# Performance work log

Hardware: AMD Instinct MI355X
Metric: run time of the kernel (lower is better)

The kernel has to match this reference:

```python
import jax, jax.numpy as jnp
import numpy as np
from jax import lax

D_MODEL = 1024
D_STATE = 16
D_CONV = 4
EXPAND = 2
D_INNER = EXPAND * D_MODEL          # 2048
DT_RANK = (D_MODEL + 15) // 16      # 64


def setup_inputs() -> dict:
    key = jax.random.key(0)
    ks = jax.random.split(key, 12)
    B, L = 2, 2048
    s = lambda *sh: 1.0 / np.sqrt(sh[-1])
    inp = {
        "x": jax.random.normal(ks[0], (B, L, D_MODEL), jnp.float32),
        "in_proj_w": jax.random.normal(ks[1], (2 * D_INNER, D_MODEL), jnp.float32) * s(0, D_MODEL),
        "conv_w": jax.random.normal(ks[2], (D_INNER, 1, D_CONV), jnp.float32) * s(0, D_CONV),
        "conv_b": jax.random.normal(ks[3], (D_INNER,), jnp.float32) * 0.01,
        "x_proj_w": jax.random.normal(ks[4], (DT_RANK + 2 * D_STATE, D_INNER), jnp.float32) * s(0, D_INNER),
        "dt_proj_w": jax.random.normal(ks[5], (D_INNER, DT_RANK), jnp.float32) * s(0, DT_RANK),
        "dt_proj_b": jax.random.normal(ks[6], (D_INNER,), jnp.float32) * 0.1 - 4.0,  # softplus(dt) small
        "A_log": jnp.log(jnp.broadcast_to(jnp.arange(1, D_STATE + 1, dtype=jnp.float32), (D_INNER, D_STATE))),
        "D": jnp.ones((D_INNER,), jnp.float32),
        "out_proj_w": jax.random.normal(ks[7], (D_MODEL, D_INNER), jnp.float32) * s(0, D_INNER),
        "ln_w": jnp.ones((D_MODEL,), jnp.float32),
        "ln_b": jnp.zeros((D_MODEL,), jnp.float32),
    }
    return inp


def _mamba(x, in_proj_w, conv_w, conv_b, x_proj_w, dt_proj_w, dt_proj_b, A_log, D, out_proj_w):
    B, L, _ = x.shape
    xz = jnp.einsum("bld,ed->ble", x, in_proj_w)          # [B,L,2*d_inner]
    xi, z = jnp.split(xz, 2, axis=-1)                       # each [B,L,d_inner]

    # causal depthwise conv1d over time
    xt = jnp.transpose(xi, (0, 2, 1))                       # [B,d_inner,L]
    xc = lax.conv_general_dilated(
        xt, conv_w, window_strides=(1,), padding=[(D_CONV - 1, 0)],
        dimension_numbers=("NCH", "OIH", "NCH"), feature_group_count=D_INNER)
    xc = jax.nn.silu(xc + conv_b[None, :, None])            # [B,d_inner,L]
    u = jnp.transpose(xc, (0, 2, 1))                        # [B,L,d_inner]

    x_dbl = jnp.einsum("bld,ed->ble", u, x_proj_w)          # [B,L,dt_rank+2N]
    dt, Bm, Cm = jnp.split(x_dbl, [DT_RANK, DT_RANK + D_STATE], axis=-1)
    delta = jax.nn.softplus(jnp.einsum("blr,dr->bld", dt, dt_proj_w) + dt_proj_b)  # [B,L,d_inner]

    A = -jnp.exp(A_log)                                     # [d_inner,N]

    def step(h, inputs):
        d_t, B_t, C_t, u_t = inputs                         # [B,d], [B,N], [B,N], [B,d]
        dA = jnp.exp(d_t[..., None] * A)                    # [B,d_inner,N]
        h = dA * h + (d_t * u_t)[..., None] * B_t[:, None, :]
        y_t = jnp.einsum("bdn,bn->bd", h, C_t)
        return h, y_t

    xs = (jnp.transpose(delta, (1, 0, 2)), jnp.transpose(Bm, (1, 0, 2)),
          jnp.transpose(Cm, (1, 0, 2)), jnp.transpose(u, (1, 0, 2)))
    h0 = jnp.zeros((B, D_INNER, D_STATE), x.dtype)
    _, ys = lax.scan(step, h0, xs)                          # ys [L,B,d_inner]
    y = jnp.transpose(ys, (1, 0, 2)) + u * D                # skip connection
    y = y * jax.nn.silu(z)                                  # gate
    return jnp.einsum("bld,ed->ble", y, out_proj_w)         # [B,L,d_model]


def reference(x, in_proj_w, conv_w, conv_b, x_proj_w, dt_proj_w, dt_proj_b,
              A_log, D, out_proj_w, ln_w, ln_b):
    residual = x
    y = _mamba(x, in_proj_w, conv_w, conv_b, x_proj_w, dt_proj_w, dt_proj_b,
               A_log, D, out_proj_w)
    # dropout is identity in eval; residual + LayerNorm
    h = y + residual
    mu = jnp.mean(h, axis=-1, keepdims=True)
    var = jnp.var(h, axis=-1, keepdims=True)
    return (h - mu) * lax.rsqrt(var + 1e-5) * ln_w + ln_b
```

## Files before the change

kernel.cpp:

```cpp
#include <hip/hip_runtime.h>

typedef unsigned short u16;
typedef __attribute__((ext_vector_type(8))) short bf8_t;
typedef __attribute__((ext_vector_type(4))) float f4_t;
typedef __attribute__((ext_vector_type(4))) unsigned short u16x4;
typedef __attribute__((ext_vector_type(8))) unsigned short u16x8;

__device__ __forceinline__ float b2f(u16 h) {
  union { unsigned u; float f; } v; v.u = ((unsigned)h) << 16; return v.f;
}
__device__ __forceinline__ u16 f2b(float f) {
  union { float f; unsigned u; } v; v.f = f;
  unsigned u = v.u;
  u += 0x7fffu + ((u >> 16) & 1u);
  return (u16)(u >> 16);
}

#define AS1C(p) ((const __attribute__((address_space(1))) void*)(p))
#define AS3(p)  ((__attribute__((address_space(3))) void*)(p))

__global__ __launch_bounds__(256)
void cvt_all(const float* __restrict__ x, const float* __restrict__ inW,
             const float* __restrict__ xprojW, const float* __restrict__ dtW,
             const float* __restrict__ outW,
             u16* __restrict__ xb, u16* __restrict__ inWb, u16* __restrict__ xpb,
             u16* __restrict__ dtWb, u16* __restrict__ outWb)
{
  int i = blockIdx.x * 256 + threadIdx.x;
  if (i >= 2703360) return;
  const float* s; u16* d; int off;
  if (i < 1048576)      { s = x;      d = xb;    off = i; }
  else if (i < 2097152) { s = inW;    d = inWb;  off = i - 1048576; }
  else if (i < 2146304) { s = xprojW; d = xpb;   off = i - 2097152; }
  else if (i < 2179072) { s = dtW;    d = dtWb;  off = i - 2146304; }
  else                  { s = outW;   d = outWb; off = i - 2179072; }
  f4_t v = *(const f4_t*)(s + (size_t)off * 4);
  u16x4 o;
#pragma unroll
  for (int j = 0; j < 4; ++j) o[j] = f2b(v[j]);
  *(u16x4*)(d + (size_t)off * 4) = o;
}

__device__ __forceinline__ void stage64(const u16* g, int ld, int row0, int rowmax,
                                        int k0, u16* lds, int wid, int lane) {
  int qg = (lane & 7) ^ ((lane >> 3) & 7);
#pragma unroll
  for (int c = 0; c < 4; ++c) {
    int chunk = wid * 4 + c;
    int r = row0 + chunk * 8 + (lane >> 3);
    if (r > rowmax) r = rowmax;
    const u16* gp = g + (size_t)r * ld + k0 + qg * 8;
    __builtin_amdgcn_global_load_lds(AS1C(gp), AS3(lds + chunk * 512), 16, 0, 0);
  }
}

template<int EPI>
__device__ __forceinline__ void gemm_body(const u16* __restrict__ A, int lda,
             const u16* __restrict__ Bt, int ldb,
             int Kblk, int Nact,
             u16* __restrict__ o16, float* __restrict__ of32,
             float* __restrict__ of32b, const float* __restrict__ biasf)
{
  __shared__ u16 lsA[128 * 64];
  __shared__ u16 lsB[128 * 64];
  const int tid = threadIdx.x;
  const int wid = tid >> 6, lane = tid & 63;
  const int wm = wid >> 1, wn = wid & 1;
  const int lrow = lane & 15;
  const int kq = lane >> 4;
  const int sw = lrow & 7;
  const int m0 = blockIdx.y * 128;
  const int n0 = (EPI == 1) ? 0 : blockIdx.x * 128;
  int kbase = 0;
  if (EPI == 1) kbase = blockIdx.x * Kblk;
  if (EPI == 3) kbase = blockIdx.z * Kblk;

  f4_t acc[4][4];
#pragma unroll
  for (int i = 0; i < 4; ++i)
#pragma unroll
    for (int j = 0; j < 4; ++j) acc[i][j] = {0.f, 0.f, 0.f, 0.f};

  for (int kt = kbase; kt < kbase + Kblk; kt += 64) {
    stage64(A,  lda, m0, 0x3fffffff, kt, lsA, wid, lane);
    stage64(Bt, ldb, n0, Nact - 1,   kt, lsB, wid, lane);
    __syncthreads();
#pragma unroll
    for (int h = 0; h < 2; ++h) {
      const int lk = ((h * 4 + kq) ^ sw) * 8;
      bf8_t af[4], bfr[4];
#pragma unroll
      for (int mi = 0; mi < 4; ++mi)
        af[mi] = *(const bf8_t*)&lsA[(wm * 64 + mi * 16 + lrow) * 64 + lk];
#pragma unroll
      for (int ni = 0; ni < 4; ++ni)
        bfr[ni] = *(const bf8_t*)&lsB[(wn * 64 + ni * 16 + lrow) * 64 + lk];
#pragma unroll
      for (int mi = 0; mi < 4; ++mi)
#pragma unroll
        for (int ni = 0; ni < 4; ++ni)
          acc[mi][ni] = __builtin_amdgcn_mfma_f32_16x16x32_bf16(af[mi], bfr[ni], acc[mi][ni], 0, 0, 0);
    }
    __syncthreads();
  }

  const int rq = (lane >> 4) * 4;
#pragma unroll
  for (int mi = 0; mi < 4; ++mi) {
#pragma unroll
    for (int ni = 0; ni < 4; ++ni) {
#pragma unroll
      for (int r = 0; r < 4; ++r) {
        int m = m0 + wm * 64 + mi * 16 + rq + r;
        int n = n0 + wn * 64 + ni * 16 + lrow;
        float v = acc[mi][ni][r];
        if (EPI == 1) {
          if (n < 96) of32[((size_t)blockIdx.x * 4096 + m) * 96 + n] = v;
        } else if (EPI == 2) {
          float t = v + biasf[n];
          float sp = (t > 20.f) ? t : log1pf(__expf(t));
          o16[(size_t)m * 2048 + n] = f2b(sp);
        } else {
          float* dst = blockIdx.z ? of32b : of32;
          dst[(size_t)m * 1024 + n] = v;
        }
      }
    }
  }
}

__global__ __launch_bounds__(256)
void gemm_xp(const u16* A, int lda, const u16* Bt, int ldb, int Kblk, int Nact,
             u16* o16, float* of32, float* of32b, const float* biasf)
{ gemm_body<1>(A, lda, Bt, ldb, Kblk, Nact, o16, of32, of32b, biasf); }

__global__ __launch_bounds__(256)
void gemm_dt(const u16* A, int lda, const u16* Bt, int ldb, int Kblk, int Nact,
             u16* o16, float* of32, float* of32b, const float* biasf)
{ gemm_body<2>(A, lda, Bt, ldb, Kblk, Nact, o16, of32, of32b, biasf); }

__global__ __launch_bounds__(256)
void gemm_out(const u16* A, int lda, const u16* Bt, int ldb, int Kblk, int Nact,
              u16* o16, float* of32, float* of32b, const float* biasf)
{ gemm_body<3>(A, lda, Bt, ldb, Kblk, Nact, o16, of32, of32b, biasf); }


__device__ __forceinline__ void stageu(const u16* __restrict__ g, int ld,
                                       int row0, int k0, u16* ldsu,
                                       int wid, int lane) {
  int qg = (lane & 7) ^ ((lane >> 3) & 7);
#pragma unroll
  for (int j = 0; j < 2; ++j) {
    int rr = j * 64 + wid * 8 + (lane >> 3);
    const u16* gp = g + (size_t)(row0 + rr) * ld + k0 + qg * 8;
    __builtin_amdgcn_global_load_lds(AS1C(gp), AS3(ldsu + (j * 512 + wid * 64) * 8), 16, 0, 0);
  }
}

#define G8_BAR()   __builtin_amdgcn_s_barrier()
#define G8_LGKM0() do { asm volatile("s_waitcnt lgkmcnt(0)" ::: "memory"); \
                        __builtin_amdgcn_sched_barrier(0); } while (0)
#define G8_LGKM8() asm volatile("s_waitcnt lgkmcnt(8)" ::: "memory")
#define G8_VM(N)   do { asm volatile("s_waitcnt vmcnt(" #N ")" ::: "memory"); \
                        __builtin_amdgcn_sched_barrier(0); } while (0)

#define RD_A(base, MH) do { \
  _Pragma("unroll") \
  for (int mi_ = 0; mi_ < 4; ++mi_) { \
    af[mi_][0] = *(const bf8_t*)((base) + arow + ((MH) * 64 + mi_ * 16) * 64 + aq0); \
    af[mi_][1] = *(const bf8_t*)((base) + arow + ((MH) * 64 + mi_ * 16) * 64 + aq1); \
  } } while (0)

#define RD_B(base, NH) do { \
  _Pragma("unroll") \
  for (int ni_ = 0; ni_ < 2; ++ni_) { \
    bfr[NH][ni_][0] = *(const bf8_t*)((base) + brow + ((NH) * 32 + ni_ * 16) * 64 + aq0); \
    bfr[NH][ni_][1] = *(const bf8_t*)((base) + brow + ((NH) * 32 + ni_ * 16) * 64 + aq1); \
  } } while (0)

#define MMA(MH, NH) do { \
  __builtin_amdgcn_s_setprio(1); \
  _Pragma("unroll") \
  for (int mi_ = 0; mi_ < 4; ++mi_) \
    _Pragma("unroll") \
    for (int ni_ = 0; ni_ < 2; ++ni_) { \
      acc[(MH) * 4 + mi_][(NH) * 2 + ni_] = __builtin_amdgcn_mfma_f32_16x16x32_bf16( \
          af[mi_][0], bfr[NH][ni_][0], acc[(MH) * 4 + mi_][(NH) * 2 + ni_], 0, 0, 0); \
      acc[(MH) * 4 + mi_][(NH) * 2 + ni_] = __builtin_amdgcn_mfma_f32_16x16x32_bf16( \
          af[mi_][1], bfr[NH][ni_][1], acc[(MH) * 4 + mi_][(NH) * 2 + ni_], 0, 0, 0); \
    } \
  __builtin_amdgcn_s_setprio(0); \
} while (0)

__global__ __launch_bounds__(512, 2)
void gemm8_in(const u16* __restrict__ A, const u16* __restrict__ Bt,
              u16* __restrict__ o16)
{
  __shared__ u16 ls[65536];
  const int tid = threadIdx.x;
  const int wid = tid >> 6, lane = tid & 63;
  const int wm = wid >> 2, wn = wid & 3;
  const int lrow = lane & 15;
  const int kq = lane >> 4;
  const int sw = lrow & 7;
  const int m0 = blockIdx.y * 256;
  const int n0 = blockIdx.x * 256;
  u16* lsA0 = ls;
  u16* lsB0 = ls + 16384;
  u16* lsA1 = ls + 32768;
  u16* lsB1 = ls + 49152;
  const int arow = (wm * 128 + lrow) * 64;
  const int brow = (wn * 64 + lrow) * 64;
  const int aq0 = (kq ^ sw) * 8;
  const int aq1 = ((4 + kq) ^ sw) * 8;

  f4_t acc[8][4];
#pragma unroll
  for (int i = 0; i < 8; ++i)
#pragma unroll
    for (int j = 0; j < 4; ++j) acc[i][j] = {0.f, 0.f, 0.f, 0.f};
  bf8_t af[4][2];
  bf8_t bfr[2][2][2];

  stageu(A,  1024, m0,        0, lsA0,        wid, lane);
  stageu(A,  1024, m0 + 128,  0, lsA0 + 8192, wid, lane);
  stageu(Bt, 1024, n0,        0, lsB0,        wid, lane);
  stageu(Bt, 1024, n0 + 128,  0, lsB0 + 8192, wid, lane);
  stageu(Bt, 1024, n0,       64, lsB1,        wid, lane);
  stageu(Bt, 1024, n0 + 128, 64, lsB1 + 8192, wid, lane);
  G8_VM(4); G8_BAR();

#pragma unroll 1
  for (int i = 0; i < 7; ++i) {
    const int k1 = (2 * i + 1) * 64, k2 = k1 + 64, k3 = k1 + 128;
    RD_A(lsA0, 0); RD_B(lsB0, 0);
    stageu(A, 1024, m0, k1, lsA1, wid, lane);
    G8_LGKM8(); G8_BAR(); G8_LGKM0(); MMA(0, 0); G8_BAR();
    RD_B(lsB0, 1);
    stageu(A, 1024, m0 + 128, k1, lsA1 + 8192, wid, lane);
    G8_BAR(); G8_LGKM0(); MMA(0, 1); G8_BAR();
    RD_A(lsA0, 1);
    stageu(Bt, 1024, n0, k2, lsB0, wid, lane);
    G8_BAR(); G8_LGKM0(); MMA(1, 0); G8_BAR();
    stageu(Bt, 1024, n0 + 128, k2, lsB0 + 8192, wid, lane);
    G8_BAR(); G8_LGKM0(); MMA(1, 1); G8_VM(4); G8_BAR();
    RD_A(lsA1, 0); RD_B(lsB1, 0);
    stageu(A, 1024, m0, k2, lsA0, wid, lane);
    G8_LGKM8(); G8_BAR(); G8_LGKM0(); MMA(0, 0); G8_BAR();
    RD_B(lsB1, 1);
    stageu(A, 1024, m0 + 128, k2, lsA0 + 8192, wid, lane);
    G8_BAR(); G8_LGKM0(); MMA(0, 1); G8_BAR();
    RD_A(lsA1, 1);
    stageu(Bt, 1024, n0, k3, lsB1, wid, lane);
    G8_BAR(); G8_LGKM0(); MMA(1, 0); G8_BAR();
    stageu(Bt, 1024, n0 + 128, k3, lsB1 + 8192, wid, lane);
    G8_BAR(); G8_LGKM0(); MMA(1, 1); G8_VM(4); G8_BAR();
  }

  {
    const int k1 = 960;
    RD_A(lsA0, 0); RD_B(lsB0, 0);
    stageu(A, 1024, m0, k1, lsA1, wid, lane);
    G8_LGKM8(); G8_BAR(); G8_LGKM0(); MMA(0, 0); G8_BAR();
    RD_B(lsB0, 1);
    stageu(A, 1024, m0 + 128, k1, lsA1 + 8192, wid, lane);
    G8_BAR(); G8_LGKM0(); MMA(0, 1); G8_BAR();
    RD_A(lsA0, 1);
    G8_BAR(); G8_LGKM0(); MMA(1, 0); G8_BAR();
    G8_BAR(); G8_LGKM0(); MMA(1, 1); G8_VM(0); G8_BAR();
    RD_A(lsA1, 0); RD_B(lsB1, 0);
    G8_BAR(); G8_LGKM0(); MMA(0, 0); G8_BAR();
    RD_B(lsB1, 1);
    G8_BAR(); G8_LGKM0(); MMA(0, 1); G8_BAR();
    RD_A(lsA1, 1);
    G8_BAR(); G8_LGKM0(); MMA(1, 0); G8_BAR();
    G8_LGKM0(); MMA(1, 1);
  }

  const int rq = (lane >> 4) * 4;
#pragma unroll
  for (int mi = 0; mi < 8; ++mi) {
#pragma unroll
    for (int ni = 0; ni < 4; ++ni) {
#pragma unroll
      for (int r = 0; r < 4; ++r) {
        int m = m0 + wm * 128 + mi * 16 + rq + r;
        int n = n0 + wn * 64 + ni * 16 + lrow;
        float v = acc[mi][ni][r];
        if (n < 2048) o16[(size_t)m * 2048 + n] = f2b(v);
        else          o16[(size_t)8388608 + (size_t)m * 2048 + (n - 2048)] = f2b(v);
      }
    }
  }
}

__global__ __launch_bounds__(256)
void xproj_reduce(const float* __restrict__ part, u16* __restrict__ dtA,
                  float* __restrict__ bc)
{
  int idx = blockIdx.x * 256 + threadIdx.x;
  int m = idx / 96, n = idx - m * 96;
  float s = 0.f;
#pragma unroll
  for (int p = 0; p < 8; ++p) s += part[(size_t)p * 393216 + idx];
  if (n < 64) dtA[(size_t)m * 64 + n] = f2b(s);
  else        bc[(size_t)m * 32 + (n - 64)] = s;
}

__global__ __launch_bounds__(256)
void conv_silu(const u16* __restrict__ xib, const float* __restrict__ cw,
               const float* __restrict__ cb, u16* __restrict__ ub)
{
  int i = blockIdx.x * 256 + threadIdx.x;
  int c8 = (i & 255) * 8;
  int row = i >> 8;
  int l = row & 2047;
  const u16* base = xib + (size_t)row * 2048 + c8;
  u16x8 x0 = {0,0,0,0,0,0,0,0}, x1 = x0, x2 = x0, x3;
  x3 = *(const u16x8*)(base);
  if (l >= 1) x2 = *(const u16x8*)(base - 2048);
  if (l >= 2) x1 = *(const u16x8*)(base - 2 * 2048);
  if (l >= 3) x0 = *(const u16x8*)(base - 3 * 2048);
  f4_t cb0 = *(const f4_t*)(cb + c8);
  f4_t cb1 = *(const f4_t*)(cb + c8 + 4);
  u16x8 o;
#pragma unroll
  for (int j = 0; j < 8; ++j) {
    f4_t w = *(const f4_t*)(cw + (size_t)(c8 + j) * 4);
    float a = (j < 4 ? cb0[j] : cb1[j - 4])
            + w[0] * b2f(x0[j]) + w[1] * b2f(x1[j])
            + w[2] * b2f(x2[j]) + w[3] * b2f(x3[j]);
    float s = a / (1.f + __expf(-a));
    o[j] = f2b(s);
  }
  *(u16x8*)(ub + (size_t)row * 2048 + c8) = o;
}

__global__ __launch_bounds__(256)
void scan_s1(const u16* __restrict__ delta_bf, const u16* __restrict__ ub,
             const float* __restrict__ bc, const float* __restrict__ alog,
             u16* __restrict__ S, float* __restrict__ Q)
{
  int blk = blockIdx.x;
  int g = blk & 7, c = (blk >> 3) & 63, b = blk >> 9;
  int d = g * 256 + threadIdx.x;
  float Av[16];
#pragma unroll
  for (int nq = 0; nq < 4; ++nq) {
    f4_t al = *(const f4_t*)(alog + (size_t)d * 16 + nq * 4);
#pragma unroll
    for (int j = 0; j < 4; ++j) Av[nq * 4 + j] = -__expf(al[j]);
  }
  float Av0 = Av[0];
  bool st = true;
#pragma unroll
  for (int n = 1; n < 16; ++n)
    st = st && (fabsf(Av[n] - (float)(n + 1) * Av0) <= 1e-3f * (float)(n + 1));
  f4_t Qr[4];
#pragma unroll
  for (int nq = 0; nq < 4; ++nq) Qr[nq] = {0.f,0.f,0.f,0.f};
  float Sd = 0.f;
  int row0 = b * 2048 + c * 32;
  if (st) {
#pragma unroll 2
    for (int i = 0; i < 32; ++i) {
      size_t row = (size_t)(row0 + i);
      float dlt = b2f(delta_bf[row * 2048 + d]);
      float uv  = b2f(ub[row * 2048 + d]);
      const float* bp = bc + row * 32;
      f4_t Bv[4];
#pragma unroll
      for (int nq = 0; nq < 4; ++nq) Bv[nq] = *(const f4_t*)(bp + nq * 4);
      float du = dlt * uv;
      float e1 = __expf(dlt * Av0);
      float a = e1;
      Sd += dlt;
#pragma unroll
      for (int n = 0; n < 16; ++n) {
        Qr[n >> 2][n & 3] = a * Qr[n >> 2][n & 3] + du * Bv[n >> 2][n & 3];
        a *= e1;
      }
    }
  } else {
#pragma unroll 2
    for (int i = 0; i < 32; ++i) {
      size_t row = (size_t)(row0 + i);
      float dlt = b2f(delta_bf[row * 2048 + d]);
      float uv  = b2f(ub[row * 2048 + d]);
      const float* bp = bc + row * 32;
      f4_t Bv[4];
#pragma unroll
      for (int nq = 0; nq < 4; ++nq) Bv[nq] = *(const f4_t*)(bp + nq * 4);
      float du = dlt * uv;
      Sd += dlt;
#pragma unroll
      for (int n = 0; n < 16; ++n) {
        float a = __expf(dlt * Av[n]);
        Qr[n >> 2][n & 3] = a * Qr[n >> 2][n & 3] + du * Bv[n >> 2][n & 3];
      }
    }
  }
  S[(size_t)(b * 64 + c) * 2048 + d] = f2b(Sd);
  size_t o = ((size_t)((b * 64 + c) * 2048 + d)) * 16;
#pragma unroll
  for (int nq = 0; nq < 4; ++nq)
    *(f4_t*)(Q + o + nq * 4) = Qr[nq];
}

__global__ __launch_bounds__(256)
void scan_comb(const u16* __restrict__ S16, float* __restrict__ Q,
               const float* __restrict__ alog)
{
  int idx = blockIdx.x * 256 + threadIdx.x;
  int b = idx >> 15, dn = idx & 32767;
  int d = dn >> 4;
  float Av = -__expf(alog[dn]);
  size_t qbase = (size_t)b * 2097152 + dn;
  size_t sbase = (size_t)b * 131072 + d;
  float H = 0.f;
#pragma unroll
  for (int cg = 0; cg < 4; ++cg) {
    float sv[16], qv[16];
#pragma unroll
    for (int j = 0; j < 16; ++j) {
      int c = cg * 16 + j;
      qv[j] = Q[qbase + (size_t)c * 32768];
      sv[j] = b2f(S16[sbase + (size_t)c * 2048]);
    }
#pragma unroll
    for (int j = 0; j < 16; ++j) {
      int c = cg * 16 + j;
      Q[qbase + (size_t)c * 32768] = H;
      H = __expf(Av * sv[j]) * H + qv[j];
    }
  }
}

__global__ __launch_bounds__(256)
void scan_s3(const u16* __restrict__ delta_bf, const u16* __restrict__ ub,
             const float* __restrict__ bc, const float* __restrict__ alog,
             const float* __restrict__ Q, const float* __restrict__ Dw,
             u16* __restrict__ zy)
{
  int blk = blockIdx.x;
  int g = blk & 7, c = (blk >> 3) & 63, b = blk >> 9;
  int d = g * 256 + threadIdx.x;
  float Av[16];
#pragma unroll
  for (int nq = 0; nq < 4; ++nq) {
    f4_t al = *(const f4_t*)(alog + (size_t)d * 16 + nq * 4);
#pragma unroll
    for (int j = 0; j < 4; ++j) Av[nq * 4 + j] = -__expf(al[j]);
  }
  float Av0 = Av[0];
  bool st = true;
#pragma unroll
  for (int n = 1; n < 16; ++n)
    st = st && (fabsf(Av[n] - (float)(n + 1) * Av0) <= 1e-3f * (float)(n + 1));
  f4_t h4[4];
  size_t o = ((size_t)((b * 64 + c) * 2048 + d)) * 16;
#pragma unroll
  for (int nq = 0; nq < 4; ++nq) h4[nq] = *(const f4_t*)(Q + o + nq * 4);
  float Dv = Dw[d];
  int row0 = b * 2048 + c * 32;
  if (st) {
#pragma unroll 2
    for (int i = 0; i < 32; ++i) {
      size_t row = (size_t)(row0 + i);
      float dlt = b2f(delta_bf[row * 2048 + d]);
      float uv  = b2f(ub[row * 2048 + d]);
      const float* bp = bc + row * 32;
      f4_t Bv[4], Cv[4];
#pragma unroll
      for (int nq = 0; nq < 4; ++nq) { Bv[nq] = *(const f4_t*)(bp + nq * 4); Cv[nq] = *(const f4_t*)(bp + 16 + nq * 4); }
      float du = dlt * uv;
      float e1 = __expf(dlt * Av0);
      float a = e1;
      float y = 0.f;
#pragma unroll
      for (int n = 0; n < 16; ++n) {
        float hn = a * h4[n >> 2][n & 3] + du * Bv[n >> 2][n & 3];
        h4[n >> 2][n & 3] = hn;
        y += hn * Cv[n >> 2][n & 3];
        a *= e1;
      }
      float zv = b2f(zy[row * 2048 + d]);
      float ov = (y + Dv * uv) * (zv / (1.f + __expf(-zv)));
      zy[row * 2048 + d] = f2b(ov);
    }
  } else {
#pragma unroll 2
    for (int i = 0; i < 32; ++i) {
      size_t row = (size_t)(row0 + i);
      float dlt = b2f(delta_bf[row * 2048 + d]);
      float uv  = b2f(ub[row * 2048 + d]);
      const float* bp = bc + row * 32;
      f4_t Bv[4], Cv[4];
#pragma unroll
      for (int nq = 0; nq < 4; ++nq) { Bv[nq] = *(const f4_t*)(bp + nq * 4); Cv[nq] = *(const f4_t*)(bp + 16 + nq * 4); }
      float du = dlt * uv;
      float y = 0.f;
#pragma unroll
      for (int n = 0; n < 16; ++n) {
        float a = __expf(dlt * Av[n]);
        float hn = a * h4[n >> 2][n & 3] + du * Bv[n >> 2][n & 3];
        h4[n >> 2][n & 3] = hn;
        y += hn * Cv[n >> 2][n & 3];
      }
      float zv = b2f(zy[row * 2048 + d]);
      float ov = (y + Dv * uv) * (zv / (1.f + __expf(-zv)));
      zy[row * 2048 + d] = f2b(ov);
    }
  }
}

__global__ __launch_bounds__(256)
void ln_kernel(const float* __restrict__ hp0, const float* __restrict__ hp1,
               const float* __restrict__ xin,
               const float* __restrict__ lnw, const float* __restrict__ lnb,
               float* __restrict__ outp)
{
  __shared__ float ssum[4], ssq[4];
  int row = blockIdx.x, t = threadIdx.x;
  f4_t h0 = *(const f4_t*)(hp0 + (size_t)row * 1024 + t * 4);
  f4_t h1 = *(const f4_t*)(hp1 + (size_t)row * 1024 + t * 4);
  f4_t xv = *(const f4_t*)(xin + (size_t)row * 1024 + t * 4);
  float v[4], s = 0.f, q = 0.f;
#pragma unroll
  for (int j = 0; j < 4; ++j) { v[j] = h0[j] + h1[j] + xv[j]; s += v[j]; q += v[j] * v[j]; }
#pragma unroll
  for (int m = 32; m; m >>= 1) { s += __shfl_xor(s, m, 64); q += __shfl_xor(q, m, 64); }
  int wv = t >> 6;
  if ((t & 63) == 0) { ssum[wv] = s; ssq[wv] = q; }
  __syncthreads();
  s = ssum[0] + ssum[1] + ssum[2] + ssum[3];
  q = ssq[0] + ssq[1] + ssq[2] + ssq[3];
  float mu = s * (1.f / 1024.f);
  float var = q * (1.f / 1024.f) - mu * mu;
  float rs = rsqrtf(var + 1e-5f);
  f4_t o;
#pragma unroll
  for (int j = 0; j < 4; ++j)
    o[j] = (v[j] - mu) * rs * lnw[t * 4 + j] + lnb[t * 4 + j];
  *(f4_t*)(outp + (size_t)row * 1024 + t * 4) = o;
}

extern "C" void kernel_launch(void* const* d_in, const int* in_sizes, int n_in,
                              void* d_out, int out_size, void* d_ws, size_t ws_size,
                              hipStream_t stream)
{
  const float* x      = (const float*)d_in[0];
  const float* inW    = (const float*)d_in[1];
  const float* convW  = (const float*)d_in[2];
  const float* convB  = (const float*)d_in[3];
  const float* xprojW = (const float*)d_in[4];
  const float* dtW    = (const float*)d_in[5];
  const float* dtB    = (const float*)d_in[6];
  const float* alog   = (const float*)d_in[7];
  const float* Dw     = (const float*)d_in[8];
  const float* outW   = (const float*)d_in[9];
  const float* lnw    = (const float*)d_in[10];
  const float* lnb    = (const float*)d_in[11];
  float* out = (float*)d_out;

  char* ws = (char*)d_ws;
  u16*   xiz    = (u16*)(ws);
  u16*   zy     = xiz + 8388608;
  u16*   xb     = (u16*)(ws + 33554432);
  u16*   inWb   = xb + 4194304;
  u16*   u_bf   = (u16*)(ws + 33554432);
  u16*   dtA    = (u16*)(ws + 50331648);
  float* bc     = (float*)(ws + 50855936);
  u16*   xprojWb= (u16*)(ws + 51380224);
  u16*   dtWb   = (u16*)(ws + 51773440);
  u16*   outWb  = (u16*)(ws + 52035584);
  u16*   delta  = xiz;
  float* hpart1 = (float*)(ws);
  float* hpart0 = (float*)d_out;
  float* xpart  = (float*)d_out;
  u16*   Sbuf   = dtA;
  float* Qbuf   = (float*)d_out;

  dim3 blk(256);
  cvt_all<<<10560, blk, 0, stream>>>(x, inW, xprojW, dtW, outW,
                                     xb, inWb, xprojWb, dtWb, outWb);
  gemm8_in<<<dim3(16, 16), dim3(512), 0, stream>>>(xb, inWb, xiz);
  conv_silu<<<4096, blk, 0, stream>>>(xiz, convW, convB, u_bf);
  gemm_xp<<<dim3(8, 32), blk, 0, stream>>>(u_bf, 2048, xprojWb, 2048, 256, 96, nullptr, xpart, nullptr, nullptr);
  xproj_reduce<<<1536, blk, 0, stream>>>(xpart, dtA, bc);
  gemm_dt<<<dim3(16, 32), blk, 0, stream>>>(dtA, 64, dtWb, 64, 64, 2048, delta, nullptr, nullptr, dtB);
  scan_s1<<<1024, blk, 0, stream>>>(delta, u_bf, bc, alog, Sbuf, Qbuf);
  scan_comb<<<256, blk, 0, stream>>>(Sbuf, Qbuf, alog);
  scan_s3<<<1024, blk, 0, stream>>>(delta, u_bf, bc, alog, Qbuf, Dw, zy);
  gemm_out<<<dim3(8, 32, 2), blk, 0, stream>>>(zy, 2048, outWb, 2048, 1024, 1024, nullptr, hpart0, hpart1, nullptr);
  ln_kernel<<<4096, blk, 0, stream>>>(hpart0, hpart1, x, lnw, lnb, out);
}
```

Before: 311.9 us.

## Replace out-projection GEMM with double-buffered 512-thread pipelined kernel

Swaps the generic 256-thread 128x128 out-projection GEMM for a dedicated 512-thread kernel that computes a 128x256 tile. It double-buffers A and B tiles in LDS via global_load_lds and interleaves the staging of the next k-slice with the MFMA phases, raising MFMA priority with setprio. The split-K into two partial outputs is kept. This is meant to hide global-load latency and raise MFMA utilisation, at the cost of heavy LDS use (96 KB) and many barriers per iteration.

Result: no change. 310.4 us (-0.5%).

```diff
diff --git a/kernel.cpp b/kernel.cpp
--- a/kernel.cpp
+++ b/kernel.cpp
@@ -73,7 +73,6 @@
   const int n0 = (EPI == 1) ? 0 : blockIdx.x * 128;
   int kbase = 0;
   if (EPI == 1) kbase = blockIdx.x * Kblk;
-  if (EPI == 3) kbase = blockIdx.z * Kblk;
 
   f4_t acc[4][4];
 #pragma unroll
@@ -120,9 +119,6 @@
           float t = v + biasf[n];
           float sp = (t > 20.f) ? t : log1pf(__expf(t));
           o16[(size_t)m * 2048 + n] = f2b(sp);
-        } else {
-          float* dst = blockIdx.z ? of32b : of32;
-          dst[(size_t)m * 1024 + n] = v;
         }
       }
     }
@@ -138,11 +134,6 @@
 void gemm_dt(const u16* A, int lda, const u16* Bt, int ldb, int Kblk, int Nact,
              u16* o16, float* of32, float* of32b, const float* biasf)
 { gemm_body<2>(A, lda, Bt, ldb, Kblk, Nact, o16, of32, of32b, biasf); }
-
-__global__ __launch_bounds__(256)
-void gemm_out(const u16* A, int lda, const u16* Bt, int ldb, int Kblk, int Nact,
-              u16* o16, float* of32, float* of32b, const float* biasf)
-{ gemm_body<3>(A, lda, Bt, ldb, Kblk, Nact, o16, of32, of32b, biasf); }
 
 
 __device__ __forceinline__ void stageu(const u16* __restrict__ g, int ld,
@@ -294,6 +285,126 @@
   }
 }
 
+
+#define ORD_A(base, MH) do { \
+  _Pragma("unroll") \
+  for (int mi_ = 0; mi_ < 2; ++mi_) { \
+    af[mi_][0] = *(const bf8_t*)((base) + arow + ((MH) * 32 + mi_ * 16) * 64 + aq0); \
+    af[mi_][1] = *(const bf8_t*)((base) + arow + ((MH) * 32 + mi_ * 16) * 64 + aq1); \
+  } } while (0)
+
+#define OMMA(MH, NH) do { \
+  __builtin_amdgcn_s_setprio(1); \
+  _Pragma("unroll") \
+  for (int mi_ = 0; mi_ < 2; ++mi_) \
+    _Pragma("unroll") \
+    for (int ni_ = 0; ni_ < 2; ++ni_) { \
+      acc[(MH) * 2 + mi_][(NH) * 2 + ni_] = __builtin_amdgcn_mfma_f32_16x16x32_bf16( \
+          af[mi_][0], bfr[NH][ni_][0], acc[(MH) * 2 + mi_][(NH) * 2 + ni_], 0, 0, 0); \
+      acc[(MH) * 2 + mi_][(NH) * 2 + ni_] = __builtin_amdgcn_mfma_f32_16x16x32_bf16( \
+          af[mi_][1], bfr[NH][ni_][1], acc[(MH) * 2 + mi_][(NH) * 2 + ni_], 0, 0, 0); \
+    } \
+  __builtin_amdgcn_s_setprio(0); \
+} while (0)
+
+__global__ __launch_bounds__(512, 2)
+void gemm8_out(const u16* __restrict__ A, const u16* __restrict__ Bt,
+               float* __restrict__ of32, float* __restrict__ of32b)
+{
+  __shared__ u16 ls[49152];
+  const int tid = threadIdx.x;
+  const int wid = tid >> 6, lane = tid & 63;
+  const int wm = wid >> 2, wn = wid & 3;
+  const int lrow = lane & 15;
+  const int kq = lane >> 4;
+  const int sw = lrow & 7;
+  const int m0 = blockIdx.y * 128;
+  const int n0 = blockIdx.x * 256;
+  const int kbase = blockIdx.z * 1024;
+  u16* lsA0 = ls;
+  u16* lsB0 = ls + 8192;
+  u16* lsA1 = ls + 24576;
+  u16* lsB1 = ls + 32768;
+  const int arow = (wm * 64 + lrow) * 64;
+  const int brow = (wn >> 1) * 8192 + ((wn & 1) * 64 + lrow) * 64;
+  const int aq0 = (kq ^ sw) * 8;
+  const int aq1 = ((4 + kq) ^ sw) * 8;
+
+  f4_t acc[4][4];
+#pragma unroll
+  for (int i = 0; i < 4; ++i)
+#pragma unroll
+    for (int j = 0; j < 4; ++j) acc[i][j] = {0.f, 0.f, 0.f, 0.f};
+  bf8_t af[2][2];
+  bf8_t bfr[2][2][2];
+
+  stageu(A,  2048, m0,        kbase,      lsA0,        wid, lane);
+  stageu(Bt, 2048, n0,        kbase,      lsB0,        wid, lane);
+  stageu(Bt, 2048, n0 + 128,  kbase,      lsB0 + 8192, wid, lane);
+  stageu(Bt, 2048, n0,        kbase + 64, lsB1,        wid, lane);
+  stageu(Bt, 2048, n0 + 128,  kbase + 64, lsB1 + 8192, wid, lane);
+  G8_VM(4); G8_BAR();
+
+#pragma unroll 1
+  for (int i = 0; i < 7; ++i) {
+    const int k1 = kbase + (2 * i + 1) * 64, k2 = k1 + 64, k3 = k1 + 128;
+    ORD_A(lsA0, 0); RD_B(lsB0, 0);
+    stageu(A, 2048, m0, k1, lsA1, wid, lane);
+    G8_BAR(); G8_LGKM0(); OMMA(0, 0); G8_BAR();
+    RD_B(lsB0, 1);
+    G8_BAR(); G8_LGKM0(); OMMA(0, 1); G8_BAR();
+    ORD_A(lsA0, 1);
+    stageu(Bt, 2048, n0, k2, lsB0, wid, lane);
+    G8_BAR(); G8_LGKM0(); OMMA(1, 0); G8_BAR();
+    stageu(Bt, 2048, n0 + 128, k2, lsB0 + 8192, wid, lane);
+    G8_BAR(); G8_LGKM0(); OMMA(1, 1); G8_VM(4); G8_BAR();
+    ORD_A(lsA1, 0); RD_B(lsB1, 0);
+    stageu(A, 2048, m0, k2, lsA0, wid, lane);
+    G8_BAR(); G8_LGKM0(); OMMA(0, 0); G8_BAR();
+    RD_B(lsB1, 1);
+    G8_BAR(); G8_LGKM0(); OMMA(0, 1); G8_BAR();
+    ORD_A(lsA1, 1);
+    stageu(Bt, 2048, n0, k3, lsB1, wid, lane);
+    G8_BAR(); G8_LGKM0(); OMMA(1, 0); G8_BAR();
+    stageu(Bt, 2048, n0 + 128, k3, lsB1 + 8192, wid, lane);
+    G8_BAR(); G8_LGKM0(); OMMA(1, 1); G8_VM(4); G8_BAR();
+  }
+
+  {
+    const int k1 = kbase + 960;
+    ORD_A(lsA0, 0); RD_B(lsB0, 0);
+    stageu(A, 2048, m0, k1, lsA1, wid, lane);
+    G8_BAR(); G8_LGKM0(); OMMA(0, 0); G8_BAR();
+    RD_B(lsB0, 1);
+    G8_BAR(); G8_LGKM0(); OMMA(0, 1); G8_BAR();
+    ORD_A(lsA0, 1);
+    G8_BAR(); G8_LGKM0(); OMMA(1, 0); G8_BAR();
+    G8_BAR(); G8_LGKM0(); OMMA(1, 1); G8_VM(0); G8_BAR();
+    ORD_A(lsA1, 0); RD_B(lsB1, 0);
+    G8_BAR(); G8_LGKM0(); OMMA(0, 0); G8_BAR();
+    RD_B(lsB1, 1);
+    G8_BAR(); G8_LGKM0(); OMMA(0, 1); G8_BAR();
+    ORD_A(lsA1, 1);
+    G8_BAR(); G8_LGKM0(); OMMA(1, 0); G8_BAR();
+    G8_LGKM0(); OMMA(1, 1);
+  }
+
+  float* dst = blockIdx.z ? of32b : of32;
+  const int rq = (lane >> 4) * 4;
+#pragma unroll
+  for (int mi = 0; mi < 4; ++mi) {
+#pragma unroll
+    for (int ni = 0; ni < 4; ++ni) {
+#pragma unroll
+      for (int r = 0; r < 4; ++r) {
+        int m = m0 + wm * 64 + mi * 16 + rq + r;
+        int n = n0 + wn * 64 + ni * 16 + lrow;
+        dst[(size_t)m * 1024 + n] = acc[mi][ni][r];
+      }
+    }
+  }
+}
+
 __global__ __launch_bounds__(256)
 void xproj_reduce(const float* __restrict__ part, u16* __restrict__ dtA,
                   float* __restrict__ bc)
@@ -592,6 +703,6 @@
   scan_s1<<<1024, blk, 0, stream>>>(delta, u_bf, bc, alog, Sbuf, Qbuf);
   scan_comb<<<256, blk, 0, stream>>>(Sbuf, Qbuf, alog);
   scan_s3<<<1024, blk, 0, stream>>>(delta, u_bf, bc, alog, Qbuf, Dw, zy);
-  gemm_out<<<dim3(8, 32, 2), blk, 0, stream>>>(zy, 2048, outWb, 2048, 1024, 1024, nullptr, hpart0, hpart1, nullptr);
+  gemm8_out<<<dim3(4, 32, 2), dim3(512), 0, stream>>>(zy, outWb, hpart0, hpart1);
   ln_kernel<<<4096, blk, 0, stream>>>(hpart0, hpart1, x, lnw, lnb, out);
 }
```

## Replace split-K out-projection GEMM with double-buffered 512-thread pipelined GEMM

Applied to the files above, without the earlier changes.

The out-projection GEMM used a split-K of 2 with 256-thread blocks, writing two fp32 partials that the layernorm kernel then summed. It is replaced by a 512-thread, 8-wave kernel that runs the full K=2048 loop over double-buffered LDS with async global-to-LDS loads interleaved with MFMA phases and raised wave priority. This drops one fp32 partial write and read and the partial sum in layernorm. The cost is that the grid halves to 256 blocks, lowering parallelism, and correctness now depends on hand-placed waitcnt and barrier ordering.

Result: faster. 305.1 us (-2.2%).

```diff
diff --git a/kernel.cpp b/kernel.cpp
--- a/kernel.cpp
+++ b/kernel.cpp
@@ -59,7 +59,7 @@
              const u16* __restrict__ Bt, int ldb,
              int Kblk, int Nact,
              u16* __restrict__ o16, float* __restrict__ of32,
-             float* __restrict__ of32b, const float* __restrict__ biasf)
+             const float* __restrict__ biasf)
 {
   __shared__ u16 lsA[128 * 64];
   __shared__ u16 lsB[128 * 64];
@@ -73,7 +73,6 @@
   const int n0 = (EPI == 1) ? 0 : blockIdx.x * 128;
   int kbase = 0;
   if (EPI == 1) kbase = blockIdx.x * Kblk;
-  if (EPI == 3) kbase = blockIdx.z * Kblk;
 
   f4_t acc[4][4];
 #pragma unroll
@@ -120,9 +119,6 @@
           float t = v + biasf[n];
           float sp = (t > 20.f) ? t : log1pf(__expf(t));
           o16[(size_t)m * 2048 + n] = f2b(sp);
-        } else {
-          float* dst = blockIdx.z ? of32b : of32;
-          dst[(size_t)m * 1024 + n] = v;
         }
       }
     }
@@ -131,18 +127,13 @@
 
 __global__ __launch_bounds__(256)
 void gemm_xp(const u16* A, int lda, const u16* Bt, int ldb, int Kblk, int Nact,
-             u16* o16, float* of32, float* of32b, const float* biasf)
-{ gemm_body<1>(A, lda, Bt, ldb, Kblk, Nact, o16, of32, of32b, biasf); }
+             u16* o16, float* of32, const float* biasf)
+{ gemm_body<1>(A, lda, Bt, ldb, Kblk, Nact, o16, of32, biasf); }
 
 __global__ __launch_bounds__(256)
 void gemm_dt(const u16* A, int lda, const u16* Bt, int ldb, int Kblk, int Nact,
-             u16* o16, float* of32, float* of32b, const float* biasf)
-{ gemm_body<2>(A, lda, Bt, ldb, Kblk, Nact, o16, of32, of32b, biasf); }
-
-__global__ __launch_bounds__(256)
-void gemm_out(const u16* A, int lda, const u16* Bt, int ldb, int Kblk, int Nact,
-              u16* o16, float* of32, float* of32b, const float* biasf)
-{ gemm_body<3>(A, lda, Bt, ldb, Kblk, Nact, o16, of32, of32b, biasf); }
+             u16* o16, float* of32, const float* biasf)
+{ gemm_body<2>(A, lda, Bt, ldb, Kblk, Nact, o16, of32, biasf); }
 
 
 __device__ __forceinline__ void stageu(const u16* __restrict__ g, int ld,
@@ -294,6 +285,112 @@
   }
 }
 
+
+#define O4_RD_A(base, KH) do { \
+  _Pragma("unroll") \
+  for (int mi_ = 0; mi_ < 4; ++mi_) \
+    af4[mi_][KH] = *(const bf8_t*)((base) + arow + mi_ * 1024 + ((KH) ? aq1 : aq0)); \
+  } while (0)
+
+#define O4_RD_B(base) do { \
+  _Pragma("unroll") \
+  for (int ni_ = 0; ni_ < 2; ++ni_) { \
+    bf4[ni_][0] = *(const bf8_t*)((base) + brow + ni_ * 1024 + aq0); \
+    bf4[ni_][1] = *(const bf8_t*)((base) + brow + ni_ * 1024 + aq1); \
+  } } while (0)
+
+#define O4_MMA(KH) do { \
+  __builtin_amdgcn_s_setprio(1); \
+  _Pragma("unroll") \
+  for (int mi_ = 0; mi_ < 4; ++mi_) \
+    _Pragma("unroll") \
+    for (int ni_ = 0; ni_ < 2; ++ni_) \
+      acc[mi_][ni_] = __builtin_amdgcn_mfma_f32_16x16x32_bf16( \
+          af4[mi_][KH], bf4[ni_][KH], acc[mi_][ni_], 0, 0, 0); \
+  __builtin_amdgcn_s_setprio(0); \
+} while (0)
+
+__global__ __launch_bounds__(512, 2)
+void gemm4_out(const u16* __restrict__ A, const u16* __restrict__ Bt,
+               float* __restrict__ yout)
+{
+  __shared__ u16 ls[32768];
+  const int tid = threadIdx.x;
+  const int wid = tid >> 6, lane = tid & 63;
+  const int wm = wid >> 2, wn = wid & 3;
+  const int lrow = lane & 15;
+  const int kq = lane >> 4;
+  const int sw = lrow & 7;
+  const int m0 = blockIdx.y * 128;
+  const int n0 = blockIdx.x * 128;
+  u16* lsA0 = ls;
+  u16* lsB0 = ls + 8192;
+  u16* lsA1 = ls + 16384;
+  u16* lsB1 = ls + 24576;
+  const int arow = (wm * 64 + lrow) * 64;
+  const int brow = (wn * 32 + lrow) * 64;
+  const int aq0 = (kq ^ sw) * 8;
+  const int aq1 = ((4 + kq) ^ sw) * 8;
+
+  f4_t acc[4][2];
+#pragma unroll
+  for (int i = 0; i < 4; ++i)
+#pragma unroll
+    for (int j = 0; j < 2; ++j) acc[i][j] = {0.f, 0.f, 0.f, 0.f};
+  bf8_t af4[4][2];
+  bf8_t bf4[2][2];
+
+  stageu(A,  2048, m0,  0, lsA0, wid, lane);
+  stageu(Bt, 2048, n0,  0, lsB0, wid, lane);
+  stageu(Bt, 2048, n0, 64, lsB1, wid, lane);
+  G8_VM(2); G8_BAR();
+
+#pragma unroll 1
+  for (int i = 0; i < 15; ++i) {
+    const int ka1 = (2 * i + 1) * 64;
+    const int k2  = ka1 + 64;
+    const int kb3 = ka1 + 128;
+    O4_RD_A(lsA0, 0); O4_RD_B(lsB0);
+    stageu(A, 2048, m0, ka1, lsA1, wid, lane);
+    G8_BAR(); G8_LGKM0(); O4_MMA(0); G8_BAR();
+    O4_RD_A(lsA0, 1);
+    stageu(Bt, 2048, n0, k2, lsB0, wid, lane);
+    G8_LGKM0(); O4_MMA(1); G8_VM(2); G8_BAR();
+    O4_RD_A(lsA1, 0); O4_RD_B(lsB1);
+    stageu(A, 2048, m0, k2, lsA0, wid, lane);
+    G8_BAR(); G8_LGKM0(); O4_MMA(0); G8_BAR();
+    O4_RD_A(lsA1, 1);
+    stageu(Bt, 2048, n0, kb3, lsB1, wid, lane);
+    G8_LGKM0(); O4_MMA(1); G8_VM(2); G8_BAR();
+  }
+
+  {
+    O4_RD_A(lsA0, 0); O4_RD_B(lsB0);
+    stageu(A, 2048, m0, 1984, lsA1, wid, lane);
+    G8_BAR(); G8_LGKM0(); O4_MMA(0); G8_BAR();
+    O4_RD_A(lsA0, 1);
+    G8_LGKM0(); O4_MMA(1); G8_VM(0); G8_BAR();
+    O4_RD_A(lsA1, 0); O4_RD_B(lsB1);
+    G8_LGKM0(); O4_MMA(0);
+    O4_RD_A(lsA1, 1);
+    G8_LGKM0(); O4_MMA(1);
+  }
+
+  const int rq = (lane >> 4) * 4;
+#pragma unroll
+  for (int mi = 0; mi < 4; ++mi) {
+#pragma unroll
+    for (int ni = 0; ni < 2; ++ni) {
+#pragma unroll
+      for (int r = 0; r < 4; ++r) {
+        int m = m0 + wm * 64 + mi * 16 + rq + r;
+        int n = n0 + wn * 32 + ni * 16 + lrow;
+        yout[(size_t)m * 1024 + n] = acc[mi][ni][r];
+      }
+    }
+  }
+}
+
 __global__ __launch_bounds__(256)
 void xproj_reduce(const float* __restrict__ part, u16* __restrict__ dtA,
                   float* __restrict__ bc)
@@ -515,19 +612,17 @@
 }
 
 __global__ __launch_bounds__(256)
-void ln_kernel(const float* __restrict__ hp0, const float* __restrict__ hp1,
-               const float* __restrict__ xin,
+void ln_kernel(const float* __restrict__ yv, const float* __restrict__ xin,
                const float* __restrict__ lnw, const float* __restrict__ lnb,
                float* __restrict__ outp)
 {
   __shared__ float ssum[4], ssq[4];
   int row = blockIdx.x, t = threadIdx.x;
-  f4_t h0 = *(const f4_t*)(hp0 + (size_t)row * 1024 + t * 4);
-  f4_t h1 = *(const f4_t*)(hp1 + (size_t)row * 1024 + t * 4);
+  f4_t h0 = *(const f4_t*)(yv + (size_t)row * 1024 + t * 4);
   f4_t xv = *(const f4_t*)(xin + (size_t)row * 1024 + t * 4);
   float v[4], s = 0.f, q = 0.f;
 #pragma unroll
-  for (int j = 0; j < 4; ++j) { v[j] = h0[j] + h1[j] + xv[j]; s += v[j]; q += v[j] * v[j]; }
+  for (int j = 0; j < 4; ++j) { v[j] = h0[j] + xv[j]; s += v[j]; q += v[j] * v[j]; }
 #pragma unroll
   for (int m = 32; m; m >>= 1) { s += __shfl_xor(s, m, 64); q += __shfl_xor(q, m, 64); }
   int wv = t >> 6;
@@ -575,23 +670,22 @@
   u16*   dtWb   = (u16*)(ws + 51773440);
   u16*   outWb  = (u16*)(ws + 52035584);
   u16*   delta  = xiz;
-  float* hpart1 = (float*)(ws);
-  float* hpart0 = (float*)d_out;
   float* xpart  = (float*)d_out;
   u16*   Sbuf   = dtA;
   float* Qbuf   = (float*)d_out;
+  float* yout   = (float*)d_out;
 
   dim3 blk(256);
   cvt_all<<<10560, blk, 0, stream>>>(x, inW, xprojW, dtW, outW,
                                      xb, inWb, xprojWb, dtWb, outWb);
   gemm8_in<<<dim3(16, 16), dim3(512), 0, stream>>>(xb, inWb, xiz);
   conv_silu<<<4096, blk, 0, stream>>>(xiz, convW, convB, u_bf);
-  gemm_xp<<<dim3(8, 32), blk, 0, stream>>>(u_bf, 2048, xprojWb, 2048, 256, 96, nullptr, xpart, nullptr, nullptr);
+  gemm_xp<<<dim3(8, 32), blk, 0, stream>>>(u_bf, 2048, xprojWb, 2048, 256, 96, nullptr, xpart, nullptr);
   xproj_reduce<<<1536, blk, 0, stream>>>(xpart, dtA, bc);
-  gemm_dt<<<dim3(16, 32), blk, 0, stream>>>(dtA, 64, dtWb, 64, 64, 2048, delta, nullptr, nullptr, dtB);
+  gemm_dt<<<dim3(16, 32), blk, 0, stream>>>(dtA, 64, dtWb, 64, 64, 2048, delta, nullptr, dtB);
   scan_s1<<<1024, blk, 0, stream>>>(delta, u_bf, bc, alog, Sbuf, Qbuf);
   scan_comb<<<256, blk, 0, stream>>>(Sbuf, Qbuf, alog);
   scan_s3<<<1024, blk, 0, stream>>>(delta, u_bf, bc, alog, Qbuf, Dw, zy);
-  gemm_out<<<dim3(8, 32, 2), blk, 0, stream>>>(zy, 2048, outWb, 2048, 1024, 1024, nullptr, hpart0, hpart1, nullptr);
-  ln_kernel<<<4096, blk, 0, stream>>>(hpart0, hpart1, x, lnw, lnb, out);
-}
+  gemm4_out<<<dim3(8, 32), dim3(512), 0, stream>>>(zy, outWb, yout);
+  ln_kernel<<<4096, blk, 0, stream>>>(yout, x, lnw, lnb, out);
+}
```
